# Kernel tuning notes

Hardware: AMD Instinct MI355X
Metric: run time of the kernel (lower is better)

## Reference

```python
import jax, jax.numpy as jnp
import numpy as np


def _lstm_layer(x_seq, W_ih, W_hh, b_ih, b_hh):
    # x_seq: (B, S, In); returns (outputs (B,S,H), h_n (B,H), c_n (B,H))
    B, S, _ = x_seq.shape
    H = W_hh.shape[1]
    # precompute the input contribution for all timesteps: (B,S,4H)
    xg = jnp.einsum('bsi,gi->bsg', x_seq, W_ih) + b_ih + b_hh
    h0 = jnp.zeros((B, H), x_seq.dtype)
    c0 = jnp.zeros((B, H), x_seq.dtype)

    def step(carry, xg_t):
        h, c = carry
        gates = xg_t + h @ W_hh.T  # (B,4H)
        i, f, g, o = jnp.split(gates, 4, axis=-1)
        i = jax.nn.sigmoid(i)
        f = jax.nn.sigmoid(f)
        g = jnp.tanh(g)
        o = jax.nn.sigmoid(o)
        c_next = f * c + i * g
        h_next = o * jnp.tanh(c_next)
        return (h_next, c_next), h_next

    (h_n, c_n), hs = jax.lax.scan(step, (h0, c0), xg.transpose(1, 0, 2))
    return hs.transpose(1, 0, 2), h_n, c_n


def setup_inputs() -> dict:
    key = jax.random.key(0)
    ks = jax.random.split(key, 5)
    B, S, I, H = 64, 1024, 256, 512
    return {
        'x': jax.random.normal(ks[0], (B, S, I), jnp.float32),
        'W_ih0': jax.random.normal(ks[1], (4 * H, I), jnp.float32) * 0.1,
        'W_hh0': jax.random.normal(ks[2], (4 * H, H), jnp.float32) * 0.1,
        'b_ih0': jnp.zeros((4 * H,), jnp.float32),
        'b_hh0': jnp.zeros((4 * H,), jnp.float32),
        'W_ih1': jax.random.normal(ks[3], (4 * H, H), jnp.float32) * 0.1,
        'W_hh1': jax.random.normal(ks[4], (4 * H, H), jnp.float32) * 0.1,
        'b_ih1': jnp.zeros((4 * H,), jnp.float32),
        'b_hh1': jnp.zeros((4 * H,), jnp.float32),
    }


def reference(x, W_ih0, W_hh0, b_ih0, b_hh0, W_ih1, W_hh1, b_ih1, b_hh1):
    # layer 0 then layer 1 (dropout=0.0, eval mode -> no-op)
    out0, h0, c0 = _lstm_layer(x, W_ih0, W_hh0, b_ih0, b_hh0)
    out1, h1, c1 = _lstm_layer(out0, W_ih1, W_hh1, b_ih1, b_hh1)
    h_n = jnp.stack([h0, h1], axis=0)  # (num_layers, B, H)
    c_n = jnp.stack([c0, c1], axis=0)
    return out1, (h_n, c_n)
```

## Files before the change

kernel.cpp:

```cpp
#include <hip/hip_runtime.h>
#include <hip/hip_bf16.h>


#define BB 64
#define SS 1024
#define HH 512
#define NWG 64

typedef unsigned short u16;
typedef __attribute__((ext_vector_type(8))) short bf16x8;
typedef __attribute__((ext_vector_type(4))) float f32x4;

__device__ __forceinline__ bf16x8 ldfrag(const u16* p) {
  return *reinterpret_cast<const bf16x8*>(p);
}
__device__ __forceinline__ u16 f2bf(float f) {
  __hip_bfloat16 h = __float2bfloat16(f);
  return *reinterpret_cast<u16*>(&h);
}
__device__ __forceinline__ bf16x8 cvt8(const float* p) {
  const f32x4* v = reinterpret_cast<const f32x4*>(p);
  f32x4 a = v[0], b = v[1];
  bf16x8 r;
  r[0] = (short)f2bf(a[0]); r[1] = (short)f2bf(a[1]);
  r[2] = (short)f2bf(a[2]); r[3] = (short)f2bf(a[3]);
  r[4] = (short)f2bf(b[0]); r[5] = (short)f2bf(b[1]);
  r[6] = (short)f2bf(b[2]); r[7] = (short)f2bf(b[3]);
  return r;
}
__device__ __forceinline__ float sigm(float x) { return 1.0f / (1.0f + __expf(-x)); }
__device__ __forceinline__ float tanh_f(float x) { return 2.0f / (1.0f + __expf(-2.0f * x)) - 1.0f; }

template<int KIN, int LAYER, bool XF32>
__device__ __forceinline__ void run_layer(
    const void* __restrict__ xin,
    const float* __restrict__ Wih,
    const float* __restrict__ Whh,
    const float* __restrict__ bih,
    const float* __restrict__ bhh,
    float* __restrict__ outF,
    u16*   __restrict__ outB,
    float* __restrict__ hn,
    float* __restrict__ cn,
    u16* __restrict__ hbuf,
    int* flag_own,
    int* flag_dep)
{
  const int g    = blockIdx.x & (NWG - 1);
  const int g8   = g * 8;
  const int tid  = threadIdx.x;
  const int wv   = tid >> 6;
  const int lane = tid & 63;
  const int q    = lane >> 4;
  const int n16  = lane & 15;

  const int c0 = n16;
  const int c1 = 16 + n16;
  const int wrow0 = ((c0 >> 3) * HH) + g8 + (c0 & 7);
  const int wrow1 = ((c1 >> 3) * HH) + g8 + (c1 & 7);

  bf16x8 wihA[KIN / 32], wihB[KIN / 32], whhA[16], whhB[16];
#pragma unroll
  for (int ks = 0; ks < KIN / 32; ++ks) {
    wihA[ks] = cvt8(Wih + (size_t)wrow0 * KIN + ks * 32 + q * 8);
    wihB[ks] = cvt8(Wih + (size_t)wrow1 * KIN + ks * 32 + q * 8);
  }
#pragma unroll
  for (int ks = 0; ks < 16; ++ks) {
    whhA[ks] = cvt8(Whh + (size_t)wrow0 * HH + ks * 32 + q * 8);
    whhB[ks] = cvt8(Whh + (size_t)wrow1 * HH + ks * 32 + q * 8);
  }
  const float bias0 = bih[wrow0] + bhh[wrow0];
  const float bias1 = bih[wrow1] + bhh[wrow1];

  float cst[4] = {0.f, 0.f, 0.f, 0.f};

  const int arow = wv * 16 + n16;

  for (int t = 0; t < SS; ++t) {
    if (tid == 0) {
      if (t > 0) {
        while (__hip_atomic_load(&flag_own[t - 1], __ATOMIC_RELAXED,
                                 __HIP_MEMORY_SCOPE_AGENT) < NWG)
          __builtin_amdgcn_s_sleep(1);
      }
      if (LAYER == 1) {
        while (__hip_atomic_load(&flag_dep[t], __ATOMIC_RELAXED,
                                 __HIP_MEMORY_SCOPE_AGENT) < NWG)
          __builtin_amdgcn_s_sleep(1);
      }
    }
    __syncthreads();
    __builtin_amdgcn_fence(__ATOMIC_ACQUIRE, "agent");

    const u16* hread  = hbuf + (size_t)(t & 1) * (BB * HH);
    u16*       hwrite = hbuf + (size_t)((t + 1) & 1) * (BB * HH);

    f32x4 acc0 = {0.f, 0.f, 0.f, 0.f};
    f32x4 acc1 = {0.f, 0.f, 0.f, 0.f};

    if (XF32) {
      const float* xp = (const float*)xin +
                        (size_t)arow * SS * KIN + (size_t)t * KIN + q * 8;
#pragma unroll
      for (int ks = 0; ks < KIN / 32; ++ks) {
        bf16x8 a = cvt8(xp + ks * 32);
        acc0 = __builtin_amdgcn_mfma_f32_16x16x32_bf16(a, wihA[ks], acc0, 0, 0, 0);
        acc1 = __builtin_amdgcn_mfma_f32_16x16x32_bf16(a, wihB[ks], acc1, 0, 0, 0);
      }
    } else {
      const u16* xp = (const u16*)xin +
                      (size_t)arow * SS * KIN + (size_t)t * KIN + q * 8;
#pragma unroll
      for (int ks = 0; ks < KIN / 32; ++ks) {
        bf16x8 a = ldfrag(xp + ks * 32);
        acc0 = __builtin_amdgcn_mfma_f32_16x16x32_bf16(a, wihA[ks], acc0, 0, 0, 0);
        acc1 = __builtin_amdgcn_mfma_f32_16x16x32_bf16(a, wihB[ks], acc1, 0, 0, 0);
      }
    }
    const u16* hp = hread + (size_t)arow * HH + q * 8;
#pragma unroll
    for (int ks = 0; ks < 16; ++ks) {
      bf16x8 a = ldfrag(hp + ks * 32);
      acc0 = __builtin_amdgcn_mfma_f32_16x16x32_bf16(a, whhA[ks], acc0, 0, 0, 0);
      acc1 = __builtin_amdgcn_mfma_f32_16x16x32_bf16(a, whhB[ks], acc1, 0, 0, 0);
    }

    float a0[4], a1[4], p0[4], p1[4];
#pragma unroll
    for (int r = 0; r < 4; ++r) { a0[r] = acc0[r] + bias0; a1[r] = acc1[r] + bias1; }
#pragma unroll
    for (int r = 0; r < 4; ++r) {
      p0[r] = __shfl_xor(a0[r], 8, 64);
      p1[r] = __shfl_xor(a1[r], 8, 64);
    }

    if (n16 < 8) {
      const int hcol = g8 + n16;
#pragma unroll
      for (int r = 0; r < 4; ++r) {
        const int b = wv * 16 + q * 4 + r;
        float ig = sigm(a0[r]);
        float fg = sigm(p0[r]);
        float gg = tanh_f(a1[r]);
        float og = sigm(p1[r]);
        float cv = fg * cst[r] + ig * gg;
        cst[r] = cv;
        float hv = og * tanh_f(cv);
        u16 hb = f2bf(hv);
        hwrite[(size_t)b * HH + hcol] = hb;
        if (LAYER == 0) {
          outB[((size_t)b * SS + t) * HH + hcol] = hb;
        } else {
          outF[((size_t)b * SS + t) * HH + hcol] = hv;
        }
        if (t == SS - 1) {
          hn[(size_t)b * HH + hcol] = hv;
          cn[(size_t)b * HH + hcol] = cv;
        }
      }
    }

    __syncthreads();
    if (tid == 0) {
      __hip_atomic_fetch_add(&flag_own[t], 1, __ATOMIC_RELEASE,
                             __HIP_MEMORY_SCOPE_AGENT);
    }
  }
}

__global__ __launch_bounds__(256, 1) void lstm_persist(
    const float* __restrict__ x,
    const float* __restrict__ Wih0, const float* __restrict__ Whh0,
    const float* __restrict__ bih0, const float* __restrict__ bhh0,
    const float* __restrict__ Wih1, const float* __restrict__ Whh1,
    const float* __restrict__ bih1, const float* __restrict__ bhh1,
    u16* out0, float* out1, float* hn, float* cn,
    u16* hbuf, int* flags)
{
  const int layer = blockIdx.x >> 6;
  if (layer == 0) {
    run_layer<256, 0, true>(x, Wih0, Whh0, bih0, bhh0,
                            nullptr, out0, hn, cn,
                            hbuf, flags, nullptr);
  } else {
    run_layer<512, 1, false>(out0, Wih1, Whh1, bih1, bhh1,
                             out1, nullptr,
                             hn + (size_t)BB * HH, cn + (size_t)BB * HH,
                             hbuf + 2 * (size_t)BB * HH, flags + SS, flags);
  }
}

extern "C" void kernel_launch(void* const* d_in, const int* in_sizes, int n_in,
                              void* d_out, int out_size, void* d_ws, size_t ws_size,
                              hipStream_t stream) {
  const float* x    = (const float*)d_in[0];
  const float* Wih0 = (const float*)d_in[1];
  const float* Whh0 = (const float*)d_in[2];
  const float* bih0 = (const float*)d_in[3];
  const float* bhh0 = (const float*)d_in[4];
  const float* Wih1 = (const float*)d_in[5];
  const float* Whh1 = (const float*)d_in[6];
  const float* bih1 = (const float*)d_in[7];
  const float* bhh1 = (const float*)d_in[8];

  float* out  = (float*)d_out;
  float* out1 = out;
  float* hn   = out + (size_t)BB * SS * HH;
  float* cn   = hn + 2 * (size_t)BB * HH;

  char* ws = (char*)d_ws;
  const size_t out0_bytes = (size_t)BB * SS * HH * 2;
  const size_t hbuf_bytes = 4 * (size_t)BB * HH * 2;
  const size_t flag_bytes = 2 * (size_t)SS * 4;
  if (ws_size < out0_bytes + hbuf_bytes + flag_bytes) return;

  u16* out0  = (u16*)ws;
  u16* hbuf  = (u16*)(ws + out0_bytes);
  int* flags = (int*)(ws + out0_bytes + hbuf_bytes);

  hipMemsetAsync(hbuf, 0, hbuf_bytes + flag_bytes, stream);

  lstm_persist<<<dim3(2 * NWG), dim3(256), 0, stream>>>(
      x, Wih0, Whh0, bih0, bhh0, Wih1, Whh1, bih1, bhh1,
      out0, out1, hn, cn, hbuf, flags);
}
```

Before: 16.11 ms.

## Use per-wave flags, 4-slot ring buffer and coherent loads to pipeline LSTM layers

Replaces the block-wide barrier and single-thread flag polling with per-wavefront step flags, so each wave waits only on the batch rows it needs. Layer 0's hidden state goes into a 4-deep ring that layer 1 reads directly, which removes the full bf16 out0 sequence buffer. A consumer flag lets layer 0 run up to four steps ahead before it overwrites a slot. The hidden-state loads and stores now use cache-bypassing sc0/sc1 instructions, and flag reads are issued early to hide polling latency. Weights are converted to bf16 once into a per-workgroup global fragment buffer and re-read every step instead of being held in registers, which lowers register pressure but adds global/L2 traffic each step.

```diff
diff --git a/kernel.cpp b/kernel.cpp
--- a/kernel.cpp
+++ b/kernel.cpp
@@ -31,99 +31,109 @@
 __device__ __forceinline__ float sigm(float x) { return 1.0f / (1.0f + __expf(-x)); }
 __device__ __forceinline__ float tanh_f(float x) { return 2.0f / (1.0f + __expf(-2.0f * x)) - 1.0f; }
 
-template<int KIN, int LAYER, bool XF32>
-__device__ __forceinline__ void run_layer(
-    const void* __restrict__ xin,
-    const float* __restrict__ Wih,
-    const float* __restrict__ Whh,
-    const float* __restrict__ bih,
-    const float* __restrict__ bhh,
-    float* __restrict__ outF,
-    u16*   __restrict__ outB,
-    float* __restrict__ hn,
-    float* __restrict__ cn,
-    u16* __restrict__ hbuf,
-    int* flag_own,
-    int* flag_dep)
+__device__ __forceinline__ bf16x8 ldg_cv(const u16* p) {
+  bf16x8 r;
+  asm volatile("global_load_dwordx4 %0, %1, off sc0 sc1"
+               : "=v"(r) : "v"(p) : "memory");
+  return r;
+}
+__device__ __forceinline__ void stg_cv16(u16* p, u16 v) {
+  unsigned int w = v;
+  asm volatile("global_store_short %0, %1, off sc0 sc1"
+               :: "v"(p), "v"(w) : "memory");
+}
+__device__ __forceinline__ int ld_flag(int* p) {
+  return __hip_atomic_load(p, __ATOMIC_RELAXED, __HIP_MEMORY_SCOPE_AGENT);
+}
+__device__ __forceinline__ void add_flag(int* p) {
+  __hip_atomic_fetch_add(p, 1, __ATOMIC_RELAXED, __HIP_MEMORY_SCOPE_AGENT);
+}
+__device__ __forceinline__ void waitflag(int* p, int probe) {
+  if (probe >= NWG) return;
+  while (ld_flag(p) < NWG) __builtin_amdgcn_s_sleep(1);
+}
+#define VMCNT0() asm volatile("s_waitcnt vmcnt(0)" ::: "memory")
+
+#define MFMA(a, b, c) __builtin_amdgcn_mfma_f32_16x16x32_bf16((a), (b), (c), 0, 0, 0)
+
+template<int KIN>
+__device__ __forceinline__ void conv_weights(
+    const float* __restrict__ Wih, const float* __restrict__ Whh,
+    u16* __restrict__ wcg, int wrow0, int wrow1, int q, int lane, int wv)
 {
-  const int g    = blockIdx.x & (NWG - 1);
-  const int g8   = g * 8;
-  const int tid  = threadIdx.x;
-  const int wv   = tid >> 6;
+  constexpr int KITER = KIN / 32;
+  constexpr int ITERS = (KITER + 16) * 2;
+  for (int iter = wv; iter < ITERS; iter += 4) {
+    const int half = iter >> 1;
+    const int wrow = (iter & 1) ? wrow1 : wrow0;
+    const float* src = (half < KITER)
+        ? (Wih + (size_t)wrow * KIN + half * 32 + q * 8)
+        : (Whh + (size_t)wrow * HH + (half - KITER) * 32 + q * 8);
+    bf16x8 f = cvt8(src);
+    *reinterpret_cast<bf16x8*>(wcg + ((size_t)iter * 64 + lane) * 8) = f;
+  }
+}
+
+__device__ __forceinline__ void run_l0(
+    const float* __restrict__ x,
+    const float* __restrict__ Wih, const float* __restrict__ Whh,
+    const float* __restrict__ bih, const float* __restrict__ bhh,
+    float* __restrict__ hn, float* __restrict__ cn,
+    u16* __restrict__ R0, int* __restrict__ fH0, int* __restrict__ fC,
+    u16* __restrict__ wcg)
+{
+  const int g = blockIdx.x & (NWG - 1);
+  const int tid = threadIdx.x;
+  const int wv = tid >> 6;
   const int lane = tid & 63;
-  const int q    = lane >> 4;
-  const int n16  = lane & 15;
-
-  const int c0 = n16;
-  const int c1 = 16 + n16;
+  const int q = lane >> 4;
+  const int n16 = lane & 15;
+  const int g8 = g * 8;
+  const int c0 = n16, c1 = 16 + n16;
   const int wrow0 = ((c0 >> 3) * HH) + g8 + (c0 & 7);
   const int wrow1 = ((c1 >> 3) * HH) + g8 + (c1 & 7);
-
-  bf16x8 wihA[KIN / 32], wihB[KIN / 32], whhA[16], whhB[16];
-#pragma unroll
-  for (int ks = 0; ks < KIN / 32; ++ks) {
-    wihA[ks] = cvt8(Wih + (size_t)wrow0 * KIN + ks * 32 + q * 8);
-    wihB[ks] = cvt8(Wih + (size_t)wrow1 * KIN + ks * 32 + q * 8);
-  }
-#pragma unroll
-  for (int ks = 0; ks < 16; ++ks) {
-    whhA[ks] = cvt8(Whh + (size_t)wrow0 * HH + ks * 32 + q * 8);
-    whhB[ks] = cvt8(Whh + (size_t)wrow1 * HH + ks * 32 + q * 8);
-  }
+  constexpr int KIN = 256, KITER = 8;
+
+  conv_weights<KIN>(Wih, Whh, wcg, wrow0, wrow1, q, lane, wv);
+  __syncthreads();
+
   const float bias0 = bih[wrow0] + bhh[wrow0];
   const float bias1 = bih[wrow1] + bhh[wrow1];
+  const int arow = wv * 16 + n16;
+  const int hcol = g8 + n16;
 
   float cst[4] = {0.f, 0.f, 0.f, 0.f};
 
-  const int arow = wv * 16 + n16;
-
   for (int t = 0; t < SS; ++t) {
-    if (tid == 0) {
-      if (t > 0) {
-        while (__hip_atomic_load(&flag_own[t - 1], __ATOMIC_RELAXED,
-                                 __HIP_MEMORY_SCOPE_AGENT) < NWG)
-          __builtin_amdgcn_s_sleep(1);
-      }
-      if (LAYER == 1) {
-        while (__hip_atomic_load(&flag_dep[t], __ATOMIC_RELAXED,
-                                 __HIP_MEMORY_SCOPE_AGENT) < NWG)
-          __builtin_amdgcn_s_sleep(1);
-      }
-    }
-    __syncthreads();
-    __builtin_amdgcn_fence(__ATOMIC_ACQUIRE, "agent");
-
-    const u16* hread  = hbuf + (size_t)(t & 1) * (BB * HH);
-    u16*       hwrite = hbuf + (size_t)((t + 1) & 1) * (BB * HH);
+    int pC = (t >= 4) ? ld_flag(&fC[(t - 4) * 4 + wv]) : NWG;
+    int pH = (t >= 1) ? ld_flag(&fH0[(t - 1) * 4 + wv]) : NWG;
 
     f32x4 acc0 = {0.f, 0.f, 0.f, 0.f};
     f32x4 acc1 = {0.f, 0.f, 0.f, 0.f};
 
-    if (XF32) {
-      const float* xp = (const float*)xin +
-                        (size_t)arow * SS * KIN + (size_t)t * KIN + q * 8;
-#pragma unroll
-      for (int ks = 0; ks < KIN / 32; ++ks) {
-        bf16x8 a = cvt8(xp + ks * 32);
-        acc0 = __builtin_amdgcn_mfma_f32_16x16x32_bf16(a, wihA[ks], acc0, 0, 0, 0);
-        acc1 = __builtin_amdgcn_mfma_f32_16x16x32_bf16(a, wihB[ks], acc1, 0, 0, 0);
-      }
-    } else {
-      const u16* xp = (const u16*)xin +
-                      (size_t)arow * SS * KIN + (size_t)t * KIN + q * 8;
-#pragma unroll
-      for (int ks = 0; ks < KIN / 32; ++ks) {
-        bf16x8 a = ldfrag(xp + ks * 32);
-        acc0 = __builtin_amdgcn_mfma_f32_16x16x32_bf16(a, wihA[ks], acc0, 0, 0, 0);
-        acc1 = __builtin_amdgcn_mfma_f32_16x16x32_bf16(a, wihB[ks], acc1, 0, 0, 0);
-      }
-    }
-    const u16* hp = hread + (size_t)arow * HH + q * 8;
+    const float* xp = x + (size_t)arow * SS * KIN + (size_t)t * KIN + q * 8;
+#pragma unroll
+    for (int ks = 0; ks < KITER; ++ks) {
+      bf16x8 a  = cvt8(xp + ks * 32);
+      bf16x8 b0 = ldfrag(wcg + ((size_t)(2 * ks + 0) * 64 + lane) * 8);
+      bf16x8 b1 = ldfrag(wcg + ((size_t)(2 * ks + 1) * 64 + lane) * 8);
+      acc0 = MFMA(a, b0, acc0);
+      acc1 = MFMA(a, b1, acc1);
+    }
+
+    if (t >= 1) waitflag(&fH0[(t - 1) * 4 + wv], pH);
+    const u16* hr = R0 + (size_t)((t + 3) & 3) * BB * HH + (size_t)arow * HH + q * 8;
+    bf16x8 hf[16];
+#pragma unroll
+    for (int ks = 0; ks < 16; ++ks) hf[ks] = ldg_cv(hr + ks * 32);
+    VMCNT0();
+    __builtin_amdgcn_sched_barrier(0);
 #pragma unroll
     for (int ks = 0; ks < 16; ++ks) {
-      bf16x8 a = ldfrag(hp + ks * 32);
-      acc0 = __builtin_amdgcn_mfma_f32_16x16x32_bf16(a, whhA[ks], acc0, 0, 0, 0);
-      acc1 = __builtin_amdgcn_mfma_f32_16x16x32_bf16(a, whhB[ks], acc1, 0, 0, 0);
+      bf16x8 b0 = ldfrag(wcg + ((size_t)(2 * (KITER + ks) + 0) * 64 + lane) * 8);
+      bf16x8 b1 = ldfrag(wcg + ((size_t)(2 * (KITER + ks) + 1) * 64 + lane) * 8);
+      acc0 = MFMA(hf[ks], b0, acc0);
+      acc1 = MFMA(hf[ks], b1, acc1);
     }
 
     float a0[4], a1[4], p0[4], p1[4];
@@ -135,8 +145,10 @@
       p1[r] = __shfl_xor(a1[r], 8, 64);
     }
 
+    if (t >= 4) waitflag(&fC[(t - 4) * 4 + wv], pC);
+
     if (n16 < 8) {
-      const int hcol = g8 + n16;
+      u16* hw = R0 + (size_t)(t & 3) * BB * HH;
 #pragma unroll
       for (int r = 0; r < 4; ++r) {
         const int b = wv * 16 + q * 4 + r;
@@ -147,25 +159,117 @@
         float cv = fg * cst[r] + ig * gg;
         cst[r] = cv;
         float hv = og * tanh_f(cv);
-        u16 hb = f2bf(hv);
-        hwrite[(size_t)b * HH + hcol] = hb;
-        if (LAYER == 0) {
-          outB[((size_t)b * SS + t) * HH + hcol] = hb;
-        } else {
-          outF[((size_t)b * SS + t) * HH + hcol] = hv;
-        }
+        stg_cv16(hw + (size_t)b * HH + hcol, f2bf(hv));
         if (t == SS - 1) {
           hn[(size_t)b * HH + hcol] = hv;
           cn[(size_t)b * HH + hcol] = cv;
         }
       }
     }
-
-    __syncthreads();
-    if (tid == 0) {
-      __hip_atomic_fetch_add(&flag_own[t], 1, __ATOMIC_RELEASE,
-                             __HIP_MEMORY_SCOPE_AGENT);
-    }
+    VMCNT0();
+    if (lane == 0) add_flag(&fH0[t * 4 + wv]);
+  }
+}
+
+__device__ __forceinline__ void run_l1(
+    const float* __restrict__ Wih, const float* __restrict__ Whh,
+    const float* __restrict__ bih, const float* __restrict__ bhh,
+    float* __restrict__ out1, float* __restrict__ hn, float* __restrict__ cn,
+    const u16* __restrict__ R0, u16* __restrict__ R1,
+    int* __restrict__ fH0, int* __restrict__ fH1, int* __restrict__ fC,
+    u16* __restrict__ wcg)
+{
+  const int g = blockIdx.x & (NWG - 1);
+  const int tid = threadIdx.x;
+  const int wv = tid >> 6;
+  const int lane = tid & 63;
+  const int q = lane >> 4;
+  const int n16 = lane & 15;
+  const int g8 = g * 8;
+  const int c0 = n16, c1 = 16 + n16;
+  const int wrow0 = ((c0 >> 3) * HH) + g8 + (c0 & 7);
+  const int wrow1 = ((c1 >> 3) * HH) + g8 + (c1 & 7);
+  constexpr int KITER = 16;
+
+  conv_weights<512>(Wih, Whh, wcg, wrow0, wrow1, q, lane, wv);
+  __syncthreads();
+
+  const float bias0 = bih[wrow0] + bhh[wrow0];
+  const float bias1 = bih[wrow1] + bhh[wrow1];
+  const int arow = wv * 16 + n16;
+  const int hcol = g8 + n16;
+
+  float cst[4] = {0.f, 0.f, 0.f, 0.f};
+
+  for (int t = 0; t < SS; ++t) {
+    int pD = ld_flag(&fH0[t * 4 + wv]);
+    int pH = (t >= 1) ? ld_flag(&fH1[(t - 1) * 4 + wv]) : NWG;
+
+    waitflag(&fH0[t * 4 + wv], pD);
+    const u16* h0r = R0 + (size_t)(t & 3) * BB * HH + (size_t)arow * HH + q * 8;
+    bf16x8 xf[16];
+#pragma unroll
+    for (int ks = 0; ks < 16; ++ks) xf[ks] = ldg_cv(h0r + ks * 32);
+    VMCNT0();
+    if (lane == 0) add_flag(&fC[t * 4 + wv]);
+    __builtin_amdgcn_sched_barrier(0);
+
+    f32x4 acc0 = {0.f, 0.f, 0.f, 0.f};
+    f32x4 acc1 = {0.f, 0.f, 0.f, 0.f};
+#pragma unroll
+    for (int ks = 0; ks < 16; ++ks) {
+      bf16x8 b0 = ldfrag(wcg + ((size_t)(2 * ks + 0) * 64 + lane) * 8);
+      bf16x8 b1 = ldfrag(wcg + ((size_t)(2 * ks + 1) * 64 + lane) * 8);
+      acc0 = MFMA(xf[ks], b0, acc0);
+      acc1 = MFMA(xf[ks], b1, acc1);
+    }
+
+    if (t >= 1) waitflag(&fH1[(t - 1) * 4 + wv], pH);
+    const u16* h1r = R1 + (size_t)((t + 1) & 1) * BB * HH + (size_t)arow * HH + q * 8;
+    bf16x8 hf[16];
+#pragma unroll
+    for (int ks = 0; ks < 16; ++ks) hf[ks] = ldg_cv(h1r + ks * 32);
+    VMCNT0();
+    __builtin_amdgcn_sched_barrier(0);
+#pragma unroll
+    for (int ks = 0; ks < 16; ++ks) {
+      bf16x8 b0 = ldfrag(wcg + ((size_t)(2 * (KITER + ks) + 0) * 64 + lane) * 8);
+      bf16x8 b1 = ldfrag(wcg + ((size_t)(2 * (KITER + ks) + 1) * 64 + lane) * 8);
+      acc0 = MFMA(hf[ks], b0, acc0);
+      acc1 = MFMA(hf[ks], b1, acc1);
+    }
+
+    float a0[4], a1[4], p0[4], p1[4];
+#pragma unroll
+    for (int r = 0; r < 4; ++r) { a0[r] = acc0[r] + bias0; a1[r] = acc1[r] + bias1; }
+#pragma unroll
+    for (int r = 0; r < 4; ++r) {
+      p0[r] = __shfl_xor(a0[r], 8, 64);
+      p1[r] = __shfl_xor(a1[r], 8, 64);
+    }
+
+    if (n16 < 8) {
+      u16* hw = R1 + (size_t)(t & 1) * BB * HH;
+#pragma unroll
+      for (int r = 0; r < 4; ++r) {
+        const int b = wv * 16 + q * 4 + r;
+        float ig = sigm(a0[r]);
+        float fg = sigm(p0[r]);
+        float gg = tanh_f(a1[r]);
+        float og = sigm(p1[r]);
+        float cv = fg * cst[r] + ig * gg;
+        cst[r] = cv;
+        float hv = og * tanh_f(cv);
+        stg_cv16(hw + (size_t)b * HH + hcol, f2bf(hv));
+        out1[((size_t)b * SS + t) * HH + hcol] = hv;
+        if (t == SS - 1) {
+          hn[(size_t)b * HH + hcol] = hv;
+          cn[(size_t)b * HH + hcol] = cv;
+        }
+      }
+    }
+    VMCNT0();
+    if (lane == 0) add_flag(&fH1[t * 4 + wv]);
   }
 }
 
@@ -175,19 +279,19 @@
     const float* __restrict__ bih0, const float* __restrict__ bhh0,
     const float* __restrict__ Wih1, const float* __restrict__ Whh1,
     const float* __restrict__ bih1, const float* __restrict__ bhh1,
-    u16* out0, float* out1, float* hn, float* cn,
-    u16* hbuf, int* flags)
+    float* out1, float* hn, float* cn,
+    u16* R0, u16* R1,
+    int* fH0, int* fH1, int* fC,
+    u16* wc0, u16* wc1)
 {
-  const int layer = blockIdx.x >> 6;
-  if (layer == 0) {
-    run_layer<256, 0, true>(x, Wih0, Whh0, bih0, bhh0,
-                            nullptr, out0, hn, cn,
-                            hbuf, flags, nullptr);
+  const int g = blockIdx.x & (NWG - 1);
+  if ((blockIdx.x >> 6) == 0) {
+    run_l0(x, Wih0, Whh0, bih0, bhh0, hn, cn,
+           R0, fH0, fC, wc0 + (size_t)g * 48 * 512);
   } else {
-    run_layer<512, 1, false>(out0, Wih1, Whh1, bih1, bhh1,
-                             out1, nullptr,
-                             hn + (size_t)BB * HH, cn + (size_t)BB * HH,
-                             hbuf + 2 * (size_t)BB * HH, flags + SS, flags);
+    run_l1(Wih1, Whh1, bih1, bhh1, out1,
+           hn + (size_t)BB * HH, cn + (size_t)BB * HH,
+           R0, R1, fH0, fH1, fC, wc1 + (size_t)g * 64 * 512);
   }
 }
 
@@ -210,18 +314,24 @@
   float* cn   = hn + 2 * (size_t)BB * HH;
 
   char* ws = (char*)d_ws;
-  const size_t out0_bytes = (size_t)BB * SS * HH * 2;
-  const size_t hbuf_bytes = 4 * (size_t)BB * HH * 2;
-  const size_t flag_bytes = 2 * (size_t)SS * 4;
-  if (ws_size < out0_bytes + hbuf_bytes + flag_bytes) return;
-
-  u16* out0  = (u16*)ws;
-  u16* hbuf  = (u16*)(ws + out0_bytes);
-  int* flags = (int*)(ws + out0_bytes + hbuf_bytes);
-
-  hipMemsetAsync(hbuf, 0, hbuf_bytes + flag_bytes, stream);
+  const size_t R0_B  = 4ull * BB * HH * 2;
+  const size_t R1_B  = 2ull * BB * HH * 2;
+  const size_t F_B   = 3ull * SS * 4 * 4;
+  const size_t WC0_B = (size_t)NWG * 48 * 512 * 2;
+  const size_t WC1_B = (size_t)NWG * 64 * 512 * 2;
+  if (ws_size < R0_B + R1_B + F_B + WC0_B + WC1_B) return;
+
+  u16* R0  = (u16*)ws;
+  u16* R1  = (u16*)(ws + R0_B);
+  int* fH0 = (int*)(ws + R0_B + R1_B);
+  int* fH1 = fH0 + SS * 4;
+  int* fC  = fH1 + SS * 4;
+  u16* wc0 = (u16*)(ws + R0_B + R1_B + F_B);
+  u16* wc1 = wc0 + (size_t)NWG * 48 * 512;
+
+  hipMemsetAsync(ws, 0, R0_B + R1_B + F_B, stream);
 
   lstm_persist<<<dim3(2 * NWG), dim3(256), 0, stream>>>(
       x, Wih0, Whh0, bih0, bhh0, Wih1, Whh1, bih1, bhh1,
-      out0, out1, hn, cn, hbuf, flags);
-}
+      out1, hn, cn, R0, R1, fH0, fH1, fC, wc0, wc1);
+}
```

Measured after the change: 21.99 ms. 36.5% more time.
